# Kernel tuning notes

Hardware: AMD Instinct MI355X
Metric: run time of the kernel (lower is better)

## Reference

```python
import jax, jax.numpy as jnp
import numpy as np

N_PILLARS_X = 512
N_PILLARS_Y = 512
N_POINTS = 1_000_000
C_GRID = 64
C_PC = 64


def setup_inputs() -> dict:
    key = jax.random.key(0)
    k1, k2, k3, k4, k5, k6, k7 = jax.random.split(key, 7)
    grid_flow_embeddings = jax.random.normal(k1, (C_GRID, N_PILLARS_X, N_PILLARS_Y), dtype=jnp.float32)
    point_cloud = jax.random.normal(k2, (N_POINTS, C_PC), dtype=jnp.float32)
    grid_indices = jax.random.randint(k3, (N_POINTS,), 0, N_PILLARS_X * N_PILLARS_Y, dtype=jnp.int64)
    Y_w = jax.random.normal(k4, (32, 128), dtype=jnp.float32) * 0.05
    Y_b = jax.random.normal(k5, (32,), dtype=jnp.float32) * 0.05
    Z_w = jax.random.normal(k6, (3, 32), dtype=jnp.float32) * 0.05
    Z_b = jax.random.normal(k7, (3,), dtype=jnp.float32) * 0.05
    return {
        "grid_flow_embeddings": grid_flow_embeddings,
        "point_cloud": point_cloud,
        "grid_indices": grid_indices,
        "Y_w": Y_w,
        "Y_b": Y_b,
        "Z_w": Z_w,
        "Z_b": Z_b,
    }


def reference(grid_flow_embeddings, point_cloud, grid_indices, Y_w, Y_b, Z_w, Z_b):
    C = grid_flow_embeddings.shape[0]
    # (C, X, Y) -> (X*Y, C): the sparse one-hot matmul is exactly a row gather
    grid_flat = grid_flow_embeddings.reshape(C, -1).T  # [X*Y, C]
    point_embeddings = jnp.take(grid_flat, grid_indices, axis=0)  # [N, C]
    full = jnp.concatenate([point_embeddings, point_cloud], axis=1)  # [N, 128]
    h = full @ Y_w.T + Y_b  # [N, 32]
    out = h @ Z_w.T + Z_b   # [N, 3]
    return out
```

## Files before the change

kernel.cpp:

```cpp
#include <hip/hip_runtime.h>
#include <stdint.h>
#include <stddef.h>

#define NCELLS (512 * 512)
#define CG 64
#define CPC 64
#define CIN 128
#define CH 32
#define COUT 3


typedef float f32x4 __attribute__((ext_vector_type(4)));

__device__ inline f32x4 nt_load4(const float* p) {
    return __builtin_nontemporal_load((const f32x4*)p);
}

__global__ void prep_kernel(const float* __restrict__ Yw,
                            const float* __restrict__ Yb,
                            const float* __restrict__ Zw,
                            const float* __restrict__ Zb,
                            const unsigned long long* __restrict__ idx_as_u64,
                            float4* __restrict__ Wemb4,
                            float4* __restrict__ Wpc4,
                            float4* __restrict__ beff,
                            int* __restrict__ flag_is64) {
    int c = threadIdx.x;
    if (c < CIN) {
        float w0 = 0.f, w1 = 0.f, w2 = 0.f;
#pragma unroll
        for (int j = 0; j < CH; ++j) {
            float y = Yw[j * CIN + c];
            w0 = fmaf(Zw[0 * CH + j], y, w0);
            w1 = fmaf(Zw[1 * CH + j], y, w1);
            w2 = fmaf(Zw[2 * CH + j], y, w2);
        }
        float4 v = make_float4(w0, w1, w2, 0.f);
        if (c < CG) Wemb4[c] = v;
        else        Wpc4[c - CG] = v;
    }
    if (c == 0) {
        float b0 = Zb[0], b1 = Zb[1], b2 = Zb[2];
#pragma unroll
        for (int j = 0; j < CH; ++j) {
            float y = Yb[j];
            b0 = fmaf(Zw[0 * CH + j], y, b0);
            b1 = fmaf(Zw[1 * CH + j], y, b1);
            b2 = fmaf(Zw[2 * CH + j], y, b2);
        }
        *beff = make_float4(b0, b1, b2, 0.f);

        int is64 = 1;
        for (int i = 0; i < 8; ++i) {
            if (idx_as_u64[i] >= (unsigned long long)NCELLS) { is64 = 0; break; }
        }
        *flag_is64 = is64;
    }
}

__global__ void __launch_bounds__(256)
gz_kernel(const float* __restrict__ grid,
          const float4* __restrict__ Wemb4,
          const float4* __restrict__ beff,
          float4* __restrict__ GZ4) {
    int p = blockIdx.x * blockDim.x + threadIdx.x;
    if (p >= NCELLS) return;

    float4 b = *beff;
    float a0 = b.x, a1 = b.y, a2 = b.z;

#pragma unroll 8
    for (int c = 0; c < CG; ++c) {
        float g = __builtin_nontemporal_load(grid + (size_t)c * NCELLS + p);
        float4 w = Wemb4[c];
        a0 = fmaf(w.x, g, a0);
        a1 = fmaf(w.y, g, a1);
        a2 = fmaf(w.z, g, a2);
    }
    GZ4[p] = make_float4(a0, a1, a2, 0.f);
}

__global__ void __launch_bounds__(256)
main_kernel(const float4* __restrict__ GZ4,
            const float* __restrict__ pc,
            const void* __restrict__ idx_raw,
            const float4* __restrict__ Wpc4,
            const int* __restrict__ flag_is64,
            float* __restrict__ out, int N) {
    const int tid = blockIdx.x * blockDim.x + threadIdx.x;
    const int ls  = threadIdx.x & 7;
    const int gstride = (gridDim.x * blockDim.x) >> 3;
    const int is64 = *flag_is64;

    const float4 wA0 = Wpc4[4 * ls + 0];
    const float4 wA1 = Wpc4[4 * ls + 1];
    const float4 wA2 = Wpc4[4 * ls + 2];
    const float4 wA3 = Wpc4[4 * ls + 3];
    const float4 wB0 = Wpc4[32 + 4 * ls + 0];
    const float4 wB1 = Wpc4[32 + 4 * ls + 1];
    const float4 wB2 = Wpc4[32 + 4 * ls + 2];
    const float4 wB3 = Wpc4[32 + 4 * ls + 3];

#pragma unroll 2
    for (int p = tid >> 3; p < N; p += gstride) {
        float gzx = 0.f, gzy = 0.f, gzz = 0.f;
        if (ls == 0) {
            int idx;
            if (is64) idx = (int)__builtin_nontemporal_load((const long long*)idx_raw + p);
            else      idx = __builtin_nontemporal_load((const int*)idx_raw + p);
            float4 gz = GZ4[idx];
            gzx = gz.x; gzy = gz.y; gzz = gz.z;
        }

        const float* prow = pc + (size_t)p * CPC;
        f32x4 x0 = nt_load4(prow + 4 * ls);
        f32x4 x1 = nt_load4(prow + 32 + 4 * ls);

        float a0, a1, a2;
        a0 = wA0.x * x0.x;            a1 = wA0.y * x0.x;            a2 = wA0.z * x0.x;
        a0 = fmaf(wA1.x, x0.y, a0);   a1 = fmaf(wA1.y, x0.y, a1);   a2 = fmaf(wA1.z, x0.y, a2);
        a0 = fmaf(wA2.x, x0.z, a0);   a1 = fmaf(wA2.y, x0.z, a1);   a2 = fmaf(wA2.z, x0.z, a2);
        a0 = fmaf(wA3.x, x0.w, a0);   a1 = fmaf(wA3.y, x0.w, a1);   a2 = fmaf(wA3.z, x0.w, a2);
        a0 = fmaf(wB0.x, x1.x, a0);   a1 = fmaf(wB0.y, x1.x, a1);   a2 = fmaf(wB0.z, x1.x, a2);
        a0 = fmaf(wB1.x, x1.y, a0);   a1 = fmaf(wB1.y, x1.y, a1);   a2 = fmaf(wB1.z, x1.y, a2);
        a0 = fmaf(wB2.x, x1.z, a0);   a1 = fmaf(wB2.y, x1.z, a1);   a2 = fmaf(wB2.z, x1.z, a2);
        a0 = fmaf(wB3.x, x1.w, a0);   a1 = fmaf(wB3.y, x1.w, a1);   a2 = fmaf(wB3.z, x1.w, a2);

#pragma unroll
        for (int m = 1; m < 8; m <<= 1) {
            a0 += __shfl_xor(a0, m, 8);
            a1 += __shfl_xor(a1, m, 8);
            a2 += __shfl_xor(a2, m, 8);
        }

        if (ls == 0) {
            float* o = out + (size_t)p * COUT;
            __builtin_nontemporal_store(a0 + gzx, o + 0);
            __builtin_nontemporal_store(a1 + gzy, o + 1);
            __builtin_nontemporal_store(a2 + gzz, o + 2);
        }
    }
}

__global__ void __launch_bounds__(256)
direct_kernel(const float* __restrict__ grid,
              const float* __restrict__ pc,
              const void* __restrict__ idx_raw,
              const float* __restrict__ Yw, const float* __restrict__ Yb,
              const float* __restrict__ Zw, const float* __restrict__ Zb,
              float* __restrict__ out, int N) {
    int i = blockIdx.x * blockDim.x + threadIdx.x;
    if (i >= N) return;
    int idx = (int)(((const long long*)idx_raw)[i]);

    float h[CH];
#pragma unroll
    for (int j = 0; j < CH; ++j) h[j] = Yb[j];
    for (int c = 0; c < CG; ++c) {
        float g = grid[(size_t)c * NCELLS + idx];
#pragma unroll
        for (int j = 0; j < CH; ++j) h[j] = fmaf(Yw[j * CIN + c], g, h[j]);
    }
    const float4* pcp = (const float4*)(pc + (size_t)i * CPC);
#pragma unroll 2
    for (int c4 = 0; c4 < CPC / 4; ++c4) {
        float4 x = pcp[c4];
#pragma unroll
        for (int j = 0; j < CH; ++j) {
            const float* w = Yw + j * CIN + CG + c4 * 4;
            h[j] = fmaf(w[0], x.x, h[j]); h[j] = fmaf(w[1], x.y, h[j]);
            h[j] = fmaf(w[2], x.z, h[j]); h[j] = fmaf(w[3], x.w, h[j]);
        }
    }
#pragma unroll
    for (int t = 0; t < COUT; ++t) {
        float a = Zb[t];
#pragma unroll
        for (int j = 0; j < CH; ++j) a = fmaf(Zw[t * CH + j], h[j], a);
        out[(size_t)i * COUT + t] = a;
    }
}

extern "C" void kernel_launch(void* const* d_in, const int* in_sizes, int n_in,
                              void* d_out, int out_size, void* d_ws, size_t ws_size,
                              hipStream_t stream) {
    const float* grid = (const float*)d_in[0];
    const float* pc   = (const float*)d_in[1];
    const void*  idx  = d_in[2];
    const float* Yw   = (const float*)d_in[3];
    const float* Yb   = (const float*)d_in[4];
    const float* Zw   = (const float*)d_in[5];
    const float* Zb   = (const float*)d_in[6];
    float* out = (float*)d_out;
    const int N = in_sizes[2];

    const size_t GZ_bytes = (size_t)NCELLS * sizeof(float4);
    const size_t W_bytes  = 64 * sizeof(float4);
    const size_t need = GZ_bytes + 2 * W_bytes + sizeof(float4) + sizeof(int);

    if (ws_size >= need) {
        char* w = (char*)d_ws;
        float4* GZ4   = (float4*)w;                       w += GZ_bytes;
        float4* Wemb4 = (float4*)w;                       w += W_bytes;
        float4* Wpc4  = (float4*)w;                       w += W_bytes;
        float4* beff  = (float4*)w;                       w += sizeof(float4);
        int*    flag  = (int*)w;

        prep_kernel<<<1, 128, 0, stream>>>(Yw, Yb, Zw, Zb,
                                           (const unsigned long long*)idx,
                                           Wemb4, Wpc4, beff, flag);
        gz_kernel<<<NCELLS / 256, 256, 0, stream>>>(grid, Wemb4, beff, GZ4);
        main_kernel<<<4096, 256, 0, stream>>>(GZ4, pc, idx, Wpc4, flag, out, N);
    } else {
        const int threads = 256;
        direct_kernel<<<(N + threads - 1) / threads, threads, 0, stream>>>(
            grid, pc, idx, Yw, Yb, Zw, Zb, out, N);
    }
}
```

Baseline: 80.32 us.

## Fuse weight prep into kernels and store grid projection as bf16

```diff
diff --git a/kernel.cpp b/kernel.cpp
--- a/kernel.cpp
+++ b/kernel.cpp
@@ -15,31 +15,38 @@
 __device__ inline f32x4 nt_load4(const float* p) {
     return __builtin_nontemporal_load((const f32x4*)p);
 }
-
-__global__ void prep_kernel(const float* __restrict__ Yw,
-                            const float* __restrict__ Yb,
-                            const float* __restrict__ Zw,
-                            const float* __restrict__ Zb,
-                            const unsigned long long* __restrict__ idx_as_u64,
-                            float4* __restrict__ Wemb4,
-                            float4* __restrict__ Wpc4,
-                            float4* __restrict__ beff,
-                            int* __restrict__ flag_is64) {
-    int c = threadIdx.x;
-    if (c < CIN) {
+__device__ inline unsigned int pack2_bf16_rne(float a, float b) {
+    unsigned int ua = __float_as_uint(a);
+    unsigned int ub = __float_as_uint(b);
+    ua = (ua + 0x7fffu + ((ua >> 16) & 1u)) >> 16;
+    ub = (ub + 0x7fffu + ((ub >> 16) & 1u)) >> 16;
+    return ua | (ub << 16);
+}
+__device__ inline float bf16_lo(unsigned int v) { return __uint_as_float(v << 16); }
+__device__ inline float bf16_hi(unsigned int v) { return __uint_as_float(v & 0xffff0000u); }
+
+__global__ void __launch_bounds__(256)
+gz_kernel(const float* __restrict__ grid,
+          const float* __restrict__ Yw,
+          const float* __restrict__ Yb,
+          const float* __restrict__ Zw,
+          const float* __restrict__ Zb,
+          uint2* __restrict__ GZ8) {
+    __shared__ float4 sW[CG];
+    __shared__ float  sB[3];
+    const int t = threadIdx.x;
+
+    if (t < CG) {
         float w0 = 0.f, w1 = 0.f, w2 = 0.f;
 #pragma unroll
         for (int j = 0; j < CH; ++j) {
-            float y = Yw[j * CIN + c];
+            float y = Yw[j * CIN + t];
             w0 = fmaf(Zw[0 * CH + j], y, w0);
             w1 = fmaf(Zw[1 * CH + j], y, w1);
             w2 = fmaf(Zw[2 * CH + j], y, w2);
         }
-        float4 v = make_float4(w0, w1, w2, 0.f);
-        if (c < CG) Wemb4[c] = v;
-        else        Wpc4[c - CG] = v;
-    }
-    if (c == 0) {
+        sW[t] = make_float4(w0, w1, w2, 0.f);
+    } else if (t == CG) {
         float b0 = Zb[0], b1 = Zb[1], b2 = Zb[2];
 #pragma unroll
         for (int j = 0; j < CH; ++j) {
@@ -48,68 +55,78 @@
             b1 = fmaf(Zw[1 * CH + j], y, b1);
             b2 = fmaf(Zw[2 * CH + j], y, b2);
         }
-        *beff = make_float4(b0, b1, b2, 0.f);
-
-        int is64 = 1;
-        for (int i = 0; i < 8; ++i) {
-            if (idx_as_u64[i] >= (unsigned long long)NCELLS) { is64 = 0; break; }
-        }
-        *flag_is64 = is64;
-    }
-}
-
-__global__ void __launch_bounds__(256)
-gz_kernel(const float* __restrict__ grid,
-          const float4* __restrict__ Wemb4,
-          const float4* __restrict__ beff,
-          float4* __restrict__ GZ4) {
-    int p = blockIdx.x * blockDim.x + threadIdx.x;
-    if (p >= NCELLS) return;
-
-    float4 b = *beff;
-    float a0 = b.x, a1 = b.y, a2 = b.z;
+        sB[0] = b0; sB[1] = b1; sB[2] = b2;
+    }
+    __syncthreads();
+
+    const int p = blockIdx.x * 256 + t;
+    float a0 = sB[0], a1 = sB[1], a2 = sB[2];
 
 #pragma unroll 8
     for (int c = 0; c < CG; ++c) {
         float g = __builtin_nontemporal_load(grid + (size_t)c * NCELLS + p);
-        float4 w = Wemb4[c];
+        float4 w = sW[c];
         a0 = fmaf(w.x, g, a0);
         a1 = fmaf(w.y, g, a1);
         a2 = fmaf(w.z, g, a2);
     }
-    GZ4[p] = make_float4(a0, a1, a2, 0.f);
+    GZ8[p] = make_uint2(pack2_bf16_rne(a0, a1), pack2_bf16_rne(a2, 0.f));
 }
 
 __global__ void __launch_bounds__(256)
-main_kernel(const float4* __restrict__ GZ4,
+main_kernel(const uint2* __restrict__ GZ8,
             const float* __restrict__ pc,
             const void* __restrict__ idx_raw,
-            const float4* __restrict__ Wpc4,
-            const int* __restrict__ flag_is64,
+            const float* __restrict__ Yw,
+            const float* __restrict__ Zw,
             float* __restrict__ out, int N) {
-    const int tid = blockIdx.x * blockDim.x + threadIdx.x;
-    const int ls  = threadIdx.x & 7;
+    __shared__ float4 sW[CG];
+    __shared__ int    sFlag;
+    const int t = threadIdx.x;
+
+    if (t < CG) {
+        float w0 = 0.f, w1 = 0.f, w2 = 0.f;
+#pragma unroll
+        for (int j = 0; j < CH; ++j) {
+            float y = Yw[j * CIN + CG + t];
+            w0 = fmaf(Zw[0 * CH + j], y, w0);
+            w1 = fmaf(Zw[1 * CH + j], y, w1);
+            w2 = fmaf(Zw[2 * CH + j], y, w2);
+        }
+        sW[t] = make_float4(w0, w1, w2, 0.f);
+    } else if (t == CG) {
+        int is64 = 1;
+        for (int i = 0; i < 8; ++i) {
+            if (((const unsigned long long*)idx_raw)[i] >= (unsigned long long)NCELLS) {
+                is64 = 0; break;
+            }
+        }
+        sFlag = is64;
+    }
+    __syncthreads();
+
+    const int ls = t & 7;
+    const int tid = blockIdx.x * blockDim.x + t;
     const int gstride = (gridDim.x * blockDim.x) >> 3;
-    const int is64 = *flag_is64;
-
-    const float4 wA0 = Wpc4[4 * ls + 0];
-    const float4 wA1 = Wpc4[4 * ls + 1];
-    const float4 wA2 = Wpc4[4 * ls + 2];
-    const float4 wA3 = Wpc4[4 * ls + 3];
-    const float4 wB0 = Wpc4[32 + 4 * ls + 0];
-    const float4 wB1 = Wpc4[32 + 4 * ls + 1];
-    const float4 wB2 = Wpc4[32 + 4 * ls + 2];
-    const float4 wB3 = Wpc4[32 + 4 * ls + 3];
+    const int is64 = sFlag;
+
+    const float4 wA0 = sW[4 * ls + 0];
+    const float4 wA1 = sW[4 * ls + 1];
+    const float4 wA2 = sW[4 * ls + 2];
+    const float4 wA3 = sW[4 * ls + 3];
+    const float4 wB0 = sW[32 + 4 * ls + 0];
+    const float4 wB1 = sW[32 + 4 * ls + 1];
+    const float4 wB2 = sW[32 + 4 * ls + 2];
+    const float4 wB3 = sW[32 + 4 * ls + 3];
 
 #pragma unroll 2
     for (int p = tid >> 3; p < N; p += gstride) {
-        float gzx = 0.f, gzy = 0.f, gzz = 0.f;
+        uint2 gz8 = make_uint2(0u, 0u);
         if (ls == 0) {
             int idx;
             if (is64) idx = (int)__builtin_nontemporal_load((const long long*)idx_raw + p);
             else      idx = __builtin_nontemporal_load((const int*)idx_raw + p);
-            float4 gz = GZ4[idx];
-            gzx = gz.x; gzy = gz.y; gzz = gz.z;
+            gz8 = GZ8[idx];
         }
 
         const float* prow = pc + (size_t)p * CPC;
@@ -135,9 +152,9 @@
 
         if (ls == 0) {
             float* o = out + (size_t)p * COUT;
-            __builtin_nontemporal_store(a0 + gzx, o + 0);
-            __builtin_nontemporal_store(a1 + gzy, o + 1);
-            __builtin_nontemporal_store(a2 + gzz, o + 2);
+            __builtin_nontemporal_store(a0 + bf16_lo(gz8.x), o + 0);
+            __builtin_nontemporal_store(a1 + bf16_hi(gz8.x), o + 1);
+            __builtin_nontemporal_store(a2 + bf16_lo(gz8.y), o + 2);
         }
     }
 }
@@ -194,23 +211,12 @@
     float* out = (float*)d_out;
     const int N = in_sizes[2];
 
-    const size_t GZ_bytes = (size_t)NCELLS * sizeof(float4);
-    const size_t W_bytes  = 64 * sizeof(float4);
-    const size_t need = GZ_bytes + 2 * W_bytes + sizeof(float4) + sizeof(int);
-
-    if (ws_size >= need) {
-        char* w = (char*)d_ws;
-        float4* GZ4   = (float4*)w;                       w += GZ_bytes;
-        float4* Wemb4 = (float4*)w;                       w += W_bytes;
-        float4* Wpc4  = (float4*)w;                       w += W_bytes;
-        float4* beff  = (float4*)w;                       w += sizeof(float4);
-        int*    flag  = (int*)w;
-
-        prep_kernel<<<1, 128, 0, stream>>>(Yw, Yb, Zw, Zb,
-                                           (const unsigned long long*)idx,
-                                           Wemb4, Wpc4, beff, flag);
-        gz_kernel<<<NCELLS / 256, 256, 0, stream>>>(grid, Wemb4, beff, GZ4);
-        main_kernel<<<4096, 256, 0, stream>>>(GZ4, pc, idx, Wpc4, flag, out, N);
+    const size_t GZ_bytes = (size_t)NCELLS * sizeof(uint2);
+
+    if (ws_size >= GZ_bytes && N >= 16) {
+        uint2* GZ8 = (uint2*)d_ws;
+        gz_kernel<<<NCELLS / 256, 256, 0, stream>>>(grid, Yw, Yb, Zw, Zb, GZ8);
+        main_kernel<<<4096, 256, 0, stream>>>(GZ8, pc, idx, Yw, Zw, out, N);
     } else {
         const int threads = 256;
         direct_kernel<<<(N + threads - 1) / threads, threads, 0, stream>>>(
```

After: 80.81 us. About the same (+0.6%).
